# Optimization experiments

Measured on AMD Instinct MI355X. Metric: run time of the kernel, lower is better.

Reference implementation:

```python
import jax, jax.numpy as jnp
import numpy as np

VOC = 32000
D = 512          # embedding_dim == hidden_dim
POS = 1024       # position_embeddings_count


def _layernorm(x, gamma, beta, eps=1e-5):
    mu = jnp.mean(x, axis=-1, keepdims=True)
    var = jnp.var(x, axis=-1, keepdims=True)
    return (x - mu) * jax.lax.rsqrt(var + eps) * gamma + beta


def setup_inputs() -> dict:
    key = jax.random.key(0)
    ks = jax.random.split(key, 7)
    inp = jax.random.randint(ks[0], (32, 1024), 0, VOC)
    word_emb = jax.random.normal(ks[1], (VOC, D), dtype=jnp.float32) * 0.02
    pos_emb = jax.random.normal(ks[2], (POS, D), dtype=jnp.float32) * 0.02
    gamma = jnp.ones((D,), dtype=jnp.float32)
    beta = jnp.zeros((D,), dtype=jnp.float32)
    # torch.rand -> uniform [0,1) init in the original Attention module
    Wk = jax.random.uniform(ks[3], (D, D), dtype=jnp.float32)
    Wq = jax.random.uniform(ks[4], (D, D), dtype=jnp.float32)
    Wv = jax.random.uniform(ks[5], (D, D), dtype=jnp.float32)
    return {"input": inp, "word_emb": word_emb, "pos_emb": pos_emb,
            "gamma": gamma, "beta": beta, "Wk": Wk, "Wq": Wq, "Wv": Wv}


def reference(input, word_emb, pos_emb, gamma, beta, Wk, Wq, Wv):
    S = input.shape[-1]
    # MiniBertEmbedding: word + positional, then LayerNorm
    emb = word_emb[input] + pos_emb[:S][None, :, :]   # [B,S,D]
    x = _layernorm(emb, gamma, beta)
    # Attention: single-head QK^T softmax V with param matrices
    k = jnp.einsum('bsd,dh->bsh', x, Wk)
    q = jnp.einsum('bsd,dh->bsh', x, Wq)
    v = jnp.einsum('bsd,do->bso', x, Wv)
    qk = jnp.einsum('bqh,bkh->bqk', q, k) / jnp.sqrt(jnp.float32(D))
    attn = jax.nn.softmax(qk, axis=-1)
    return jnp.einsum('bqk,bko->bqo', attn, v)
```

## Files before the change

### kernel.cpp

```cpp
#include <hip/hip_runtime.h>
#include <math.h>

typedef _Float16 f16;
typedef _Float16 half8 __attribute__((ext_vector_type(8)));
typedef _Float16 hv2 __attribute__((ext_vector_type(2)));
typedef _Float16 hv4 __attribute__((ext_vector_type(4)));
typedef float f32x4 __attribute__((ext_vector_type(4)));
typedef __attribute__((address_space(1))) const unsigned int gu32;
typedef __attribute__((address_space(3))) unsigned int lu32;

#define BB 32
#define SS 1024
#define DD 512
#define NR (BB*SS)
#define CH 16

__device__ __forceinline__ void stage128(const char* g, int ldb, char* lds,
                                         int wv, int ln) {
  #pragma unroll
  for (int r = 0; r < 4; r++) {
    int slot = r * 256 + wv * 64 + ln;
    int row = slot >> 3, cp = slot & 7;
    int c = cp ^ (row & 7);
    const char* gp = g + (size_t)row * ldb + (c << 4);
    char* lp = lds + ((slot - ln) << 4);
    __builtin_amdgcn_global_load_lds((gu32*)gp, (lu32*)lp, 16, 0, 0);
  }
}

__device__ __forceinline__ void stage8k_512(const char* g, int ldb, char* lds) {
  int tid = threadIdx.x;
  int slot = tid;
  int row = slot >> 3, cp = slot & 7;
  int c = cp ^ (row & 7);
  const char* gp = g + (size_t)row * ldb + (c << 4);
  char* lp = lds + ((slot - (tid & 63)) << 4);
  __builtin_amdgcn_global_load_lds((gu32*)gp, (lu32*)lp, 16, 0, 0);
}

__device__ __forceinline__ void stage16k_512(const char* g, int ldb, char* lds) {
  int tid = threadIdx.x;
  #pragma unroll
  for (int r = 0; r < 2; r++) {
    int slot = r * 512 + tid;
    int row = slot >> 3, cp = slot & 7;
    int c = cp ^ (row & 7);
    const char* gp = g + (size_t)row * ldb + (c << 4);
    char* lp = lds + ((slot - (tid & 63)) << 4);
    __builtin_amdgcn_global_load_lds((gu32*)gp, (lu32*)lp, 16, 0, 0);
  }
}

__device__ __forceinline__ void stageB32(const f16* X, size_t rowbase, int k0,
                                         char* Bset) {
  int tid = threadIdx.x;
  int q4 = tid >> 7;
  int inner = tid & 127;
  char* lds = Bset + q4 * 4096;
  const char* g = (const char*)(X + (rowbase + (size_t)q4 * 256) * DD + k0);
  #pragma unroll
  for (int r = 0; r < 2; r++) {
    int slot = r * 128 + inner;
    int row = slot >> 3, cp = slot & 7;
    int c = cp ^ (row & 7);
    const char* gp = g + (size_t)row * 1024 + (c << 4);
    char* lp = lds + ((slot - (tid & 63)) << 4);
    __builtin_amdgcn_global_load_lds((gu32*)gp, (lu32*)lp, 16, 0, 0);
  }
}

__device__ __forceinline__ half8 frag_ld(const char* lds, int row, int kc) {
  return *(const half8*)(lds + row * 128 + ((kc ^ (row & 7)) << 4));
}

__device__ __forceinline__ f32x4 MF(half8 a, half8 b, f32x4 c) {
  return __builtin_amdgcn_mfma_f32_16x16x32_f16(a, b, c, 0, 0, 0);
}

__global__ __launch_bounds__(256) void k_prep(
    const int* __restrict__ inp, const float* __restrict__ wemb,
    const float* __restrict__ pemb, const float* __restrict__ gamma,
    const float* __restrict__ beta, f16* __restrict__ Xhi, f16* __restrict__ Xlo,
    const float* __restrict__ Wq, const float* __restrict__ Wk,
    const float* __restrict__ Wv, f16* __restrict__ Wqh, f16* __restrict__ Wql,
    f16* __restrict__ Wkh, f16* __restrict__ Wkl, f16* __restrict__ Wvt)
{
  int bid = blockIdx.x;
  int tid = threadIdx.x;
  __shared__ float red[10];
  __shared__ float Lt[64][65];
  if (bid >= NR) {
    int t  = bid - NR;
    int mz = t >> 6;
    int tt = t & 63;
    if (mz < 2) {
      const float* W = mz ? Wk : Wq;
      f16* Oh = mz ? Wkh : Wqh;
      f16* Ol = mz ? Wkl : Wql;
      #pragma unroll
      for (int p = 0; p < 4; p++) {
        size_t base = (size_t)tt * 4096 + p * 1024 + tid * 4;
        float4 v = *(const float4*)&W[base];
        f16 h0 = (f16)v.x, h1 = (f16)v.y, h2 = (f16)v.z, h3 = (f16)v.w;
        hv4 hi = {h0, h1, h2, h3};
        hv4 lo = {(f16)(v.x - (float)h0), (f16)(v.y - (float)h1),
                  (f16)(v.z - (float)h2), (f16)(v.w - (float)h3)};
        *(hv4*)&Oh[base] = hi;
        *(hv4*)&Ol[base] = lo;
      }
      return;
    }
    int tr = tt >> 3, tc = tt & 7;
    int rr = tid >> 4;
    int c4 = (tid & 15) * 4;
    #pragma unroll
    for (int p = 0; p < 4; p++) {
      float4 v = *(const float4*)&Wv[(size_t)(tr * 64 + p * 16 + rr) * DD + tc * 64 + c4];
      Lt[p * 16 + rr][c4 + 0] = v.x; Lt[p * 16 + rr][c4 + 1] = v.y;
      Lt[p * 16 + rr][c4 + 2] = v.z; Lt[p * 16 + rr][c4 + 3] = v.w;
    }
    __syncthreads();
    #pragma unroll
    for (int p = 0; p < 4; p++) {
      int dl = p * 16 + rr;
      float v0 = Lt[c4 + 0][dl], v1 = Lt[c4 + 1][dl];
      float v2 = Lt[c4 + 2][dl], v3 = Lt[c4 + 3][dl];
      size_t o = (size_t)(tc * 64 + dl) * DD + tr * 64 + c4;
      *(hv4*)&Wvt[o] = (hv4){(f16)v0, (f16)v1, (f16)v2, (f16)v3};
    }
    return;
  }
  int row = bid;
  int s   = row & (SS - 1);
  int tok = inp[row];
  float2 w = ((const float2*)(wemb + (size_t)tok * DD))[tid];
  float2 p = ((const float2*)(pemb + (size_t)s   * DD))[tid];
  float ex = w.x + p.x, ey = w.y + p.y;
  float sum = ex + ey, ssq = ex*ex + ey*ey;
  #pragma unroll
  for (int off = 32; off > 0; off >>= 1) {
    sum += __shfl_down(sum, off, 64);
    ssq += __shfl_down(ssq, off, 64);
  }
  int wv = tid >> 6, ln = tid & 63;
  if (ln == 0) { red[wv] = sum; red[4 + wv] = ssq; }
  __syncthreads();
  if (tid == 0) {
    float s4 = red[0] + red[1] + red[2] + red[3];
    float q4 = red[4] + red[5] + red[6] + red[7];
    float mean = s4 * (1.0f / DD);
    float var  = q4 * (1.0f / DD) - mean * mean;
    red[8] = mean; red[9] = rsqrtf(var + 1e-5f);
  }
  __syncthreads();
  float mean = red[8], rstd = red[9];
  float2 g  = ((const float2*)gamma)[tid];
  float2 bt = ((const float2*)beta)[tid];
  float ox = (ex - mean) * rstd * g.x + bt.x;
  float oy = (ey - mean) * rstd * g.y + bt.y;
  f16 hx = (f16)ox, hy = (f16)oy;
  f16 lx = (f16)(ox - (float)hx), ly = (f16)(oy - (float)hy);
  ((hv2*)(Xhi + (size_t)row * DD))[tid] = (hv2){hx, hy};
  ((hv2*)(Xlo + (size_t)row * DD))[tid] = (hv2){lx, ly};
}

__global__ __launch_bounds__(256, 2) void k_mt(
    const f16* __restrict__ Wkh, const f16* __restrict__ Wkl,
    const f16* __restrict__ Wqh, const f16* __restrict__ Wql,
    f16* __restrict__ Mthi, f16* __restrict__ Mtlo)
{
  __shared__ __align__(16) char Ah[16384], Al[16384], Bh[16384], Bl[16384];
  int tid = threadIdx.x, wv = tid >> 6, ln = tid & 63;
  int mw = wv & 1, nw = wv >> 1;
  int n0 = blockIdx.x * 128;
  int m0 = blockIdx.y * 128;
  f32x4 acc[4][4];
  #pragma unroll
  for (int i = 0; i < 4; i++)
    #pragma unroll
    for (int j = 0; j < 4; j++) acc[i][j] = (f32x4)(0.0f);
  int quad = ln >> 4, l15 = ln & 15;
  for (int k0 = 0; k0 < DD; k0 += 64) {
    __syncthreads();
    stage128((const char*)(Wkh + (size_t)m0 * DD + k0), 1024, Ah, wv, ln);
    stage128((const char*)(Wkl + (size_t)m0 * DD + k0), 1024, Al, wv, ln);
    stage128((const char*)(Wqh + (size_t)n0 * DD + k0), 1024, Bh, wv, ln);
    stage128((const char*)(Wql + (size_t)n0 * DD + k0), 1024, Bl, wv, ln);
    __syncthreads();
    #pragma unroll
    for (int ks = 0; ks < 2; ks++) {
      int kc = ks * 4 + quad;
      half8 ah[4], al[4], bh[4], bl[4];
      #pragma unroll
      for (int t = 0; t < 4; t++) {
        ah[t] = frag_ld(Ah, mw * 64 + t * 16 + l15, kc);
        al[t] = frag_ld(Al, mw * 64 + t * 16 + l15, kc);
        bh[t] = frag_ld(Bh, nw * 64 + t * 16 + l15, kc);
        bl[t] = frag_ld(Bl, nw * 64 + t * 16 + l15, kc);
      }
      #pragma unroll
      for (int i = 0; i < 4; i++)
        #pragma unroll
        for (int j = 0; j < 4; j++) {
          acc[i][j] = MF(ah[i], bh[j], acc[i][j]);
          acc[i][j] = MF(ah[i], bl[j], acc[i][j]);
          acc[i][j] = MF(al[i], bh[j], acc[i][j]);
        }
    }
  }
  #pragma unroll
  for (int i = 0; i < 4; i++)
    #pragma unroll
    for (int j = 0; j < 4; j++)
      #pragma unroll
      for (int rg = 0; rg < 4; rg++) {
        int gm = m0 + mw * 64 + i * 16 + quad * 4 + rg;
        int gn = n0 + nw * 64 + j * 16 + l15;
        size_t o = (size_t)gm * DD + gn;
        float v = acc[i][j][rg];
        f16 h = (f16)v;
        Mthi[o] = h; Mtlo[o] = (f16)(v - (float)h);
      }
}

__global__ __launch_bounds__(512, 4) void k_projm(
    const f16* __restrict__ Xhi, const f16* __restrict__ Xlo,
    const f16* __restrict__ Mthi, const f16* __restrict__ Mtlo,
    f16* __restrict__ Sqhi, f16* __restrict__ Sqlo)
{
  __shared__ __align__(16) char Ah[16384], Al[16384], Bh[16384], Bl[16384];
  int tid = threadIdx.x, wv = tid >> 6, ln = tid & 63;
  int mw = wv & 1, nw = wv >> 1;
  int L = blockIdx.x;
  int xb = (L >> 3) & 3;
  int y  = ((L >> 5) << 3) + (L & 7);
  int n0 = xb * 128;
  int m0 = y * 128;
  f32x4 acc[4][2];
  #pragma unroll
  for (int i = 0; i < 4; i++)
    #pragma unroll
    for (int j = 0; j < 2; j++) acc[i][j] = (f32x4)(0.0f);
  int quad = ln >> 4, l15 = ln & 15;
  for (int k0 = 0; k0 < DD; k0 += 64) {
    __syncthreads();
    stage16k_512((const char*)(Xhi  + (size_t)m0 * DD + k0), 1024, Ah);
    stage16k_512((const char*)(Xlo  + (size_t)m0 * DD + k0), 1024, Al);
    stage16k_512((const char*)(Mthi + (size_t)n0 * DD + k0), 1024, Bh);
    stage16k_512((const char*)(Mtlo + (size_t)n0 * DD + k0), 1024, Bl);
    __syncthreads();
    #pragma unroll
    for (int ks = 0; ks < 2; ks++) {
      int kc = ks * 4 + quad;
      half8 ah[4], al[4], bh[2], bl[2];
      #pragma unroll
      for (int t = 0; t < 4; t++) {
        ah[t] = frag_ld(Ah, mw * 64 + t * 16 + l15, kc);
        al[t] = frag_ld(Al, mw * 64 + t * 16 + l15, kc);
      }
      #pragma unroll
      for (int t = 0; t < 2; t++) {
        bh[t] = frag_ld(Bh, nw * 32 + t * 16 + l15, kc);
        bl[t] = frag_ld(Bl, nw * 32 + t * 16 + l15, kc);
      }
      #pragma unroll
      for (int i = 0; i < 4; i++)
        #pragma unroll
        for (int j = 0; j < 2; j++) {
          acc[i][j] = MF(ah[i], bh[j], acc[i][j]);
          acc[i][j] = MF(ah[i], bl[j], acc[i][j]);
          acc[i][j] = MF(al[i], bh[j], acc[i][j]);
        }
    }
  }
  #pragma unroll
  for (int i = 0; i < 4; i++)
    #pragma unroll
    for (int j = 0; j < 2; j++)
      #pragma unroll
      for (int rg = 0; rg < 4; rg++) {
        int gm = m0 + mw * 64 + i * 16 + quad * 4 + rg;
        int gn = n0 + nw * 32 + j * 16 + l15;
        size_t o = (size_t)gm * DD + gn;
        float v = acc[i][j][rg];
        f16 h = (f16)v;
        Sqhi[o] = h; Sqlo[o] = (f16)(v - (float)h);
      }
}

__global__ __launch_bounds__(256, 2) void k_vt(
    const f16* __restrict__ Wvt, const f16* __restrict__ Xhi, f16* __restrict__ Vt)
{
  __shared__ __align__(16) char Ah[2][16384], Bh[2][16384];
  int tid = threadIdx.x, wv = tid >> 6, ln = tid & 63;
  int mw = wv & 1, nw = wv >> 1;
  int orig = blockIdx.x;
  int L = (orig & 7) * 128 + (orig >> 3);
  int c = L >> 7, t = L & 127;
  int m0 = (t & 3) * 128;
  int n0 = (c * 32 + (t >> 2)) * 128;
  f32x4 acc[4][4];
  #pragma unroll
  for (int i = 0; i < 4; i++)
    #pragma unroll
    for (int j = 0; j < 4; j++) acc[i][j] = (f32x4)(0.0f);
  int quad = ln >> 4, l15 = ln & 15;
  stage128((const char*)(Wvt + (size_t)m0 * DD), 1024, Ah[0], wv, ln);
  stage128((const char*)(Xhi + (size_t)n0 * DD), 1024, Bh[0], wv, ln);
  for (int k0 = 0; k0 < DD; k0 += 64) {
    int cur = (k0 >> 6) & 1;
    __builtin_amdgcn_s_barrier();
    __builtin_amdgcn_sched_barrier(0);
    if (k0 + 64 < DD) {
      stage128((const char*)(Wvt + (size_t)m0 * DD + k0 + 64), 1024, Ah[cur ^ 1], wv, ln);
      stage128((const char*)(Xhi + (size_t)n0 * DD + k0 + 64), 1024, Bh[cur ^ 1], wv, ln);
      asm volatile("s_waitcnt vmcnt(8)" ::: "memory");
    } else {
      asm volatile("s_waitcnt vmcnt(0)" ::: "memory");
    }
    __builtin_amdgcn_s_barrier();
    __builtin_amdgcn_sched_barrier(0);
    #pragma unroll
    for (int ks = 0; ks < 2; ks++) {
      int kc = ks * 4 + quad;
      half8 a[4], b[4];
      #pragma unroll
      for (int tt = 0; tt < 4; tt++) {
        a[tt] = frag_ld(Ah[cur], mw * 64 + tt * 16 + l15, kc);
        b[tt] = frag_ld(Bh[cur], nw * 64 + tt * 16 + l15, kc);
      }
      #pragma unroll
      for (int i = 0; i < 4; i++)
        #pragma unroll
        for (int j = 0; j < 4; j++) acc[i][j] = MF(a[i], b[j], acc[i][j]);
    }
  }
  #pragma unroll
  for (int i = 0; i < 4; i++)
    #pragma unroll
    for (int j = 0; j < 4; j++)
      #pragma unroll
      for (int rg = 0; rg < 4; rg++) {
        int gm = m0 + mw * 64 + i * 16 + quad * 4 + rg;
        int gn = n0 + nw * 64 + j * 16 + l15;
        Vt[(size_t)gm * NR + gn] = (f16)acc[i][j][rg];
      }
}

__global__ __launch_bounds__(512, 2) void k_qk(
    const f16* __restrict__ Sqhi, const f16* __restrict__ Sqlo,
    const f16* __restrict__ Xhi, const f16* __restrict__ Xlo,
    f16* __restrict__ Pws, f16* __restrict__ Pd)
{
  __shared__ __align__(16) char Ah[8192], Al[8192];
  __shared__ __align__(16) char Bh[2][16384], Bl[2][16384];
  int tid = threadIdx.x, wv = tid >> 6, ln = tid & 63;
  int rowg = wv & 1, qd = wv >> 1;
  int L = blockIdx.x;
  int g  = L >> 7;
  int rr = L & 127;
  int z  = g * 8 + (rr & 7);
  int m0 = (rr >> 3) * 64;
  size_t zr = (size_t)z * SS;
  f32x4 acc[2][16];
  #pragma unroll
  for (int i = 0; i < 2; i++)
    #pragma unroll
    for (int j = 0; j < 16; j++) acc[i][j] = (f32x4)(0.0f);
  int quad = ln >> 4, l15 = ln & 15;

  stage8k_512((const char*)(Sqhi + (zr + m0) * DD), 1024, Ah);
  stage8k_512((const char*)(Sqlo + (zr + m0) * DD), 1024, Al);
  stageB32(Xhi, zr + 0, 0, Bh[0]);
  stageB32(Xlo, zr + 0, 0, Bl[0]);

  half8 afh[2][2], afl[2][2];
  for (int k0 = 0; k0 < DD; k0 += 64) {
    #pragma unroll
    for (int r = 0; r < 8; r++) {
      __builtin_amdgcn_s_barrier();
      __builtin_amdgcn_sched_barrier(0);
      bool lastPhase = (k0 == DD - 64 && r == 7);
      if (!lastPhase) {
        int nk0 = (r == 7) ? k0 + 64 : k0;
        int nr  = (r + 1) & 7;
        stageB32(Xhi, zr + nr * 32, nk0, Bh[(r + 1) & 1]);
        stageB32(Xlo, zr + nr * 32, nk0, Bl[(r + 1) & 1]);
        if (r == 7) {
          stage8k_512((const char*)(Sqhi + (zr + m0) * DD + k0 + 64), 1024, Ah);
          stage8k_512((const char*)(Sqlo + (zr + m0) * DD + k0 + 64), 1024, Al);
          asm volatile("s_waitcnt vmcnt(6)" ::: "memory");
        } else {
          asm volatile("s_waitcnt vmcnt(4)" ::: "memory");
        }
      } else {
        asm volatile("s_waitcnt vmcnt(0)" ::: "memory");
      }
      __builtin_amdgcn_s_barrier();
      __builtin_amdgcn_sched_barrier(0);
      if (r == 0) {
        #pragma unroll
        for (int ks = 0; ks < 2; ks++)
          #pragma unroll
          for (int i = 0; i < 2; i++) {
            afh[ks][i] = frag_ld(Ah, rowg * 32 + i * 16 + l15, ks * 4 + quad);
            afl[ks][i] = frag_ld(Al, rowg * 32 + i * 16 + l15, ks * 4 + quad);
          }
      }
      const char* Bhc = Bh[r & 1] + qd * 4096;
      const char* Blc = Bl[r & 1] + qd * 4096;
      #pragma unroll
      for (int ks = 0; ks < 2; ks++) {
        int kc = ks * 4 + quad;
        #pragma unroll
        for (int jj = 0; jj < 2; jj++) {
          half8 bh = frag_ld(Bhc, jj * 16 + l15, kc);
          half8 bl = frag_ld(Blc, jj * 16 + l15, kc);
          #pragma unroll
          for (int i = 0; i < 2; i++) {
            acc[i][r * 2 + jj] = MF(afh[ks][i], bh, acc[i][r * 2 + jj]);
            acc[i][r * 2 + jj] = MF(afh[ks][i], bl, acc[i][r * 2 + jj]);
            acc[i][r * 2 + jj] = MF(afl[ks][i], bh, acc[i][r * 2 + jj]);
          }
        }
      }
    }
  }
  __syncthreads();
  float* redm = (float*)&Bh[0][0];
  float* reds = redm + 256;

  const float scale = 0.044194173824159216f;
  float mx[2][4];
  #pragma unroll
  for (int i = 0; i < 2; i++)
    #pragma unroll
    for (int rg = 0; rg < 4; rg++) mx[i][rg] = -3.0e38f;
  #pragma unroll
  for (int i = 0; i < 2; i++)
    #pragma unroll
    for (int j = 0; j < 16; j++)
      #pragma unroll
      for (int rg = 0; rg < 4; rg++) {
        acc[i][j][rg] *= scale;
        mx[i][rg] = fmaxf(mx[i][rg], acc[i][j][rg]);
      }
  #pragma unroll
  for (int off = 1; off < 16; off <<= 1)
    #pragma unroll
    for (int i = 0; i < 2; i++)
      #pragma unroll
      for (int rg = 0; rg < 4; rg++)
        mx[i][rg] = fmaxf(mx[i][rg], __shfl_xor(mx[i][rg], off, 64));
  if (l15 == 0) {
    #pragma unroll
    for (int i = 0; i < 2; i++)
      #pragma unroll
      for (int rg = 0; rg < 4; rg++)
        redm[qd * 64 + rowg * 32 + i * 16 + quad * 4 + rg] = mx[i][rg];
  }
  __syncthreads();
  float fm[2][4], sum[2][4];
  #pragma unroll
  for (int i = 0; i < 2; i++)
    #pragma unroll
    for (int rg = 0; rg < 4; rg++) {
      int row = rowg * 32 + i * 16 + quad * 4 + rg;
      fm[i][rg] = fmaxf(fmaxf(redm[row], redm[64 + row]),
                        fmaxf(redm[128 + row], redm[192 + row]));
      sum[i][rg] = 0.0f;
    }
  #pragma unroll
  for (int i = 0; i < 2; i++)
    #pragma unroll
    for (int j = 0; j < 16; j++)
      #pragma unroll
      for (int rg = 0; rg < 4; rg++) {
        float e = __expf(acc[i][j][rg] - fm[i][rg]);
        acc[i][j][rg] = e;
        sum[i][rg] += e;
      }
  #pragma unroll
  for (int off = 1; off < 16; off <<= 1)
    #pragma unroll
    for (int i = 0; i < 2; i++)
      #pragma unroll
      for (int rg = 0; rg < 4; rg++)
        sum[i][rg] += __shfl_xor(sum[i][rg], off, 64);
  if (l15 == 0) {
    #pragma unroll
    for (int i = 0; i < 2; i++)
      #pragma unroll
      for (int rg = 0; rg < 4; rg++)
        reds[qd * 64 + rowg * 32 + i * 16 + quad * 4 + rg] = sum[i][rg];
  }
  __syncthreads();
  float inv[2][4];
  #pragma unroll
  for (int i = 0; i < 2; i++)
    #pragma unroll
    for (int rg = 0; rg < 4; rg++) {
      int row = rowg * 32 + i * 16 + quad * 4 + rg;
      inv[i][rg] = 1.0f / (reds[row] + reds[64 + row] + reds[128 + row] + reds[192 + row]);
    }
  f16* Pb = (z < CH) ? Pws : Pd;
  size_t zo = (size_t)((z < CH) ? z : z - CH);
  #pragma unroll
  for (int i = 0; i < 2; i++)
    #pragma unroll
    for (int j = 0; j < 16; j++)
      #pragma unroll
      for (int rg = 0; rg < 4; rg++) {
        int row = rowg * 32 + i * 16 + quad * 4 + rg;
        int col = qd * 256 + j * 16 + l15;
        Pb[(zo * SS + m0 + row) * SS + col] = (f16)(acc[i][j][rg] * inv[i][rg]);
      }
}

__global__ __launch_bounds__(256, 2) void k_pv(
    const f16* __restrict__ P, const f16* __restrict__ Vt, float* __restrict__ O,
    int zoff)
{
  __shared__ __align__(16) char Ah[2][16384], Bh[2][16384];
  int tid = threadIdx.x, wv = tid >> 6, ln = tid & 63;
  int mw = wv & 1, nw = wv >> 1;
  int orig = blockIdx.x;
  int L = (orig & 7) * 64 + (orig >> 3);
  int c = L >> 6, t = L & 63;
  int zl = 2 * c + (t >> 5);
  int m0 = ((t >> 2) & 7) * 128;
  int n0 = (t & 3) * 128;
  int b  = zoff + zl;
  const char* Pt = (const char*)(P + ((size_t)zl * SS + m0) * SS);
  const char* Vb = (const char*)(Vt + (size_t)n0 * NR + (size_t)b * SS);
  f32x4 acc[4][4];
  #pragma unroll
  for (int i = 0; i < 4; i++)
    #pragma unroll
    for (int j = 0; j < 4; j++) acc[i][j] = (f32x4)(0.0f);
  int quad = ln >> 4, l15 = ln & 15;
  stage128(Pt, 2048, Ah[0], wv, ln);
  stage128(Vb, NR * 2, Bh[0], wv, ln);
  for (int k0 = 0; k0 < SS; k0 += 64) {
    int cur = (k0 >> 6) & 1;
    __builtin_amdgcn_s_barrier();
    __builtin_amdgcn_sched_barrier(0);
    if (k0 + 64 < SS) {
      stage128(Pt + (k0 + 64) * 2, 2048, Ah[cur ^ 1], wv, ln);
      stage128(Vb + (k0 + 64) * 2, NR * 2, Bh[cur ^ 1], wv, ln);
      asm volatile("s_waitcnt vmcnt(8)" ::: "memory");
    } else {
      asm volatile("s_waitcnt vmcnt(0)" ::: "memory");
    }
    __builtin_amdgcn_s_barrier();
    __builtin_amdgcn_sched_barrier(0);
    #pragma unroll
    for (int ks = 0; ks < 2; ks++) {
      int kc = ks * 4 + quad;
      half8 a[4], bf[4];
      #pragma unroll
      for (int tt = 0; tt < 4; tt++) {
        a[tt]  = frag_ld(Ah[cur], mw * 64 + tt * 16 + l15, kc);
        bf[tt] = frag_ld(Bh[cur], nw * 64 + tt * 16 + l15, kc);
      }
      #pragma unroll
      for (int i = 0; i < 4; i++)
        #pragma unroll
        for (int j = 0; j < 4; j++) acc[i][j] = MF(a[i], bf[j], acc[i][j]);
    }
  }
  #pragma unroll
  for (int i = 0; i < 4; i++)
    #pragma unroll
    for (int j = 0; j < 4; j++)
      #pragma unroll
      for (int rg = 0; rg < 4; rg++) {
        int gm = m0 + mw * 64 + i * 16 + quad * 4 + rg;
        int gn = n0 + nw * 64 + j * 16 + l15;
        O[((size_t)b * SS + gm) * DD + gn] = acc[i][j][rg];
      }
}

extern "C" void kernel_launch(void* const* d_in, const int* in_sizes, int n_in,
                              void* d_out, int out_size, void* d_ws, size_t ws_size,
                              hipStream_t stream) {
  const int*   inp   = (const int*)d_in[0];
  const float* wemb  = (const float*)d_in[1];
  const float* pemb  = (const float*)d_in[2];
  const float* gamma = (const float*)d_in[3];
  const float* beta  = (const float*)d_in[4];
  const float* Wk    = (const float*)d_in[5];
  const float* Wq    = (const float*)d_in[6];
  const float* Wv    = (const float*)d_in[7];

  char* ws = (char*)d_ws;
  f16* Xhi  = (f16*)ws;
  f16* Xlo  = (f16*)(ws + ((size_t)32 << 20));
  f16* Sqhi = (f16*)(ws + ((size_t)64 << 20));
  f16* Sqlo = (f16*)(ws + ((size_t)96 << 20));
  f16* Vt   = (f16*)(ws + ((size_t)128 << 20));
  f16* Pws  = (f16*)(ws + ((size_t)160 << 20));
  f16* Pd   = (f16*)d_out;

  f16* Wqh  = (f16*)d_out;
  f16* Wql  = Wqh + (size_t)DD * DD;
  f16* Wkh  = Wql + (size_t)DD * DD;
  f16* Wkl  = Wkh + (size_t)DD * DD;
  f16* Wvt  = Wkl + (size_t)DD * DD;
  f16* Mthi = Wvt + (size_t)DD * DD;
  f16* Mtlo = Mthi + (size_t)DD * DD;

  k_prep<<<NR + 192, 256, 0, stream>>>(inp, wemb, pemb, gamma, beta, Xhi, Xlo,
                                       Wq, Wk, Wv, Wqh, Wql, Wkh, Wkl, Wvt);
  k_mt<<<dim3(DD / 128, DD / 128), 256, 0, stream>>>(Wkh, Wkl, Wqh, Wql, Mthi, Mtlo);
  k_projm<<<1024, 512, 0, stream>>>(Xhi, Xlo, Mthi, Mtlo, Sqhi, Sqlo);
  k_vt<<<1024, 256, 0, stream>>>(Wvt, Xhi, Vt);
  k_qk<<<512, 512, 0, stream>>>(Sqhi, Sqlo, Xhi, Xlo, Pws, Pd);
  k_pv<<<512, 256, 0, stream>>>(Pd,  Vt, (float*)d_out, CH);
  k_pv<<<512, 256, 0, stream>>>(Pws, Vt, (float*)d_out, 0);
}
```

Before: 425.8 us.

## Shrink QK+softmax tile to 32 query rows with 256-thread blocks

The fused QK^T+softmax kernel now uses 256-thread blocks covering 32 query rows instead of 512-thread blocks covering 64 rows, doubling the grid to 1024 blocks. Each wave stages its own slice of the key tiles, and softmax reductions get dedicated shared arrays instead of reusing the B buffers, which removes one __syncthreads. The aim is more, smaller blocks for better load balance and scheduling flexibility. In exchange, key (X) tiles are reloaded twice as often across blocks, and each wave has more outstanding loads per phase.

```diff
diff --git a/kernel.cpp b/kernel.cpp
--- a/kernel.cpp
+++ b/kernel.cpp
@@ -28,16 +28,6 @@
   }
 }
 
-__device__ __forceinline__ void stage8k_512(const char* g, int ldb, char* lds) {
-  int tid = threadIdx.x;
-  int slot = tid;
-  int row = slot >> 3, cp = slot & 7;
-  int c = cp ^ (row & 7);
-  const char* gp = g + (size_t)row * ldb + (c << 4);
-  char* lp = lds + ((slot - (tid & 63)) << 4);
-  __builtin_amdgcn_global_load_lds((gu32*)gp, (lu32*)lp, 16, 0, 0);
-}
-
 __device__ __forceinline__ void stage16k_512(const char* g, int ldb, char* lds) {
   int tid = threadIdx.x;
   #pragma unroll
@@ -51,20 +41,28 @@
   }
 }
 
-__device__ __forceinline__ void stageB32(const f16* X, size_t rowbase, int k0,
-                                         char* Bset) {
+__device__ __forceinline__ void stageA32(const f16* Sq, size_t rowbase, int k0,
+                                         char* lds) {
   int tid = threadIdx.x;
-  int q4 = tid >> 7;
-  int inner = tid & 127;
-  char* lds = Bset + q4 * 4096;
-  const char* g = (const char*)(X + (rowbase + (size_t)q4 * 256) * DD + k0);
-  #pragma unroll
-  for (int r = 0; r < 2; r++) {
-    int slot = r * 128 + inner;
+  int slot = tid;
+  int row = slot >> 3, cp = slot & 7;
+  int c = cp ^ (row & 7);
+  const char* gp = (const char*)(Sq + (rowbase + (size_t)row) * DD + k0) + (c << 4);
+  char* lp = lds + ((slot - (tid & 63)) << 4);
+  __builtin_amdgcn_global_load_lds((gu32*)gp, (lu32*)lp, 16, 0, 0);
+}
+
+__device__ __forceinline__ void stageB32w(const f16* X, size_t rowbase, int k0,
+                                          char* BsetQd) {
+  int ln = threadIdx.x & 63;
+  const char* g = (const char*)(X + rowbase * DD + k0);
+  #pragma unroll
+  for (int r = 0; r < 4; r++) {
+    int slot = r * 64 + ln;
     int row = slot >> 3, cp = slot & 7;
     int c = cp ^ (row & 7);
     const char* gp = g + (size_t)row * 1024 + (c << 4);
-    char* lp = lds + ((slot - (tid & 63)) << 4);
+    char* lp = BsetQd + ((slot - ln) << 4);
     __builtin_amdgcn_global_load_lds((gu32*)gp, (lu32*)lp, 16, 0, 0);
   }
 }
@@ -347,21 +345,23 @@
       }
 }
 
-__global__ __launch_bounds__(512, 2) void k_qk(
+__global__ __launch_bounds__(256, 2) void k_qk(
     const f16* __restrict__ Sqhi, const f16* __restrict__ Sqlo,
     const f16* __restrict__ Xhi, const f16* __restrict__ Xlo,
     f16* __restrict__ Pws, f16* __restrict__ Pd)
 {
-  __shared__ __align__(16) char Ah[8192], Al[8192];
+  __shared__ __align__(16) char Ah[4096], Al[4096];
   __shared__ __align__(16) char Bh[2][16384], Bl[2][16384];
-  int tid = threadIdx.x, wv = tid >> 6, ln = tid & 63;
-  int rowg = wv & 1, qd = wv >> 1;
+  __shared__ float redm[4][32], reds[4][32];
+  int tid = threadIdx.x, ln = tid & 63;
+  int qd = tid >> 6;
   int L = blockIdx.x;
-  int g  = L >> 7;
-  int rr = L & 127;
+  int g  = L >> 8;
+  int rr = L & 255;
   int z  = g * 8 + (rr & 7);
-  int m0 = (rr >> 3) * 64;
+  int m0 = (rr >> 3) * 32;
   size_t zr = (size_t)z * SS;
+  size_t kb = zr + (size_t)qd * 256;
   f32x4 acc[2][16];
   #pragma unroll
   for (int i = 0; i < 2; i++)
@@ -369,10 +369,10 @@
     for (int j = 0; j < 16; j++) acc[i][j] = (f32x4)(0.0f);
   int quad = ln >> 4, l15 = ln & 15;
 
-  stage8k_512((const char*)(Sqhi + (zr + m0) * DD), 1024, Ah);
-  stage8k_512((const char*)(Sqlo + (zr + m0) * DD), 1024, Al);
-  stageB32(Xhi, zr + 0, 0, Bh[0]);
-  stageB32(Xlo, zr + 0, 0, Bl[0]);
+  stageA32(Sqhi, zr + m0, 0, Ah);
+  stageA32(Sqlo, zr + m0, 0, Al);
+  stageB32w(Xhi, kb, 0, Bh[0] + qd * 4096);
+  stageB32w(Xlo, kb, 0, Bl[0] + qd * 4096);
 
   half8 afh[2][2], afl[2][2];
   for (int k0 = 0; k0 < DD; k0 += 64) {
@@ -384,14 +384,14 @@
       if (!lastPhase) {
         int nk0 = (r == 7) ? k0 + 64 : k0;
         int nr  = (r + 1) & 7;
-        stageB32(Xhi, zr + nr * 32, nk0, Bh[(r + 1) & 1]);
-        stageB32(Xlo, zr + nr * 32, nk0, Bl[(r + 1) & 1]);
+        stageB32w(Xhi, kb + nr * 32, nk0, Bh[(r + 1) & 1] + qd * 4096);
+        stageB32w(Xlo, kb + nr * 32, nk0, Bl[(r + 1) & 1] + qd * 4096);
         if (r == 7) {
-          stage8k_512((const char*)(Sqhi + (zr + m0) * DD + k0 + 64), 1024, Ah);
-          stage8k_512((const char*)(Sqlo + (zr + m0) * DD + k0 + 64), 1024, Al);
-          asm volatile("s_waitcnt vmcnt(6)" ::: "memory");
+          stageA32(Sqhi, zr + m0, k0 + 64, Ah);
+          stageA32(Sqlo, zr + m0, k0 + 64, Al);
+          asm volatile("s_waitcnt vmcnt(10)" ::: "memory");
         } else {
-          asm volatile("s_waitcnt vmcnt(4)" ::: "memory");
+          asm volatile("s_waitcnt vmcnt(8)" ::: "memory");
         }
       } else {
         asm volatile("s_waitcnt vmcnt(0)" ::: "memory");
@@ -403,8 +403,8 @@
         for (int ks = 0; ks < 2; ks++)
           #pragma unroll
           for (int i = 0; i < 2; i++) {
-            afh[ks][i] = frag_ld(Ah, rowg * 32 + i * 16 + l15, ks * 4 + quad);
-            afl[ks][i] = frag_ld(Al, rowg * 32 + i * 16 + l15, ks * 4 + quad);
+            afh[ks][i] = frag_ld(Ah, i * 16 + l15, ks * 4 + quad);
+            afl[ks][i] = frag_ld(Al, i * 16 + l15, ks * 4 + quad);
           }
       }
       const char* Bhc = Bh[r & 1] + qd * 4096;
@@ -426,9 +426,6 @@
       }
     }
   }
-  __syncthreads();
-  float* redm = (float*)&Bh[0][0];
-  float* reds = redm + 256;
 
   const float scale = 0.044194173824159216f;
   float mx[2][4];
@@ -457,7 +454,7 @@
     for (int i = 0; i < 2; i++)
       #pragma unroll
       for (int rg = 0; rg < 4; rg++)
-        redm[qd * 64 + rowg * 32 + i * 16 + quad * 4 + rg] = mx[i][rg];
+        redm[qd][i * 16 + quad * 4 + rg] = mx[i][rg];
   }
   __syncthreads();
   float fm[2][4], sum[2][4];
@@ -465,9 +462,9 @@
   for (int i = 0; i < 2; i++)
     #pragma unroll
     for (int rg = 0; rg < 4; rg++) {
-      int row = rowg * 32 + i * 16 + quad * 4 + rg;
-      fm[i][rg] = fmaxf(fmaxf(redm[row], redm[64 + row]),
-                        fmaxf(redm[128 + row], redm[192 + row]));
+      int row = i * 16 + quad * 4 + rg;
+      fm[i][rg] = fmaxf(fmaxf(redm[0][row], redm[1][row]),
+                        fmaxf(redm[2][row], redm[3][row]));
       sum[i][rg] = 0.0f;
     }
   #pragma unroll
@@ -492,7 +489,7 @@
     for (int i = 0; i < 2; i++)
       #pragma unroll
       for (int rg = 0; rg < 4; rg++)
-        reds[qd * 64 + rowg * 32 + i * 16 + quad * 4 + rg] = sum[i][rg];
+        reds[qd][i * 16 + quad * 4 + rg] = sum[i][rg];
   }
   __syncthreads();
   float inv[2][4];
@@ -500,8 +497,8 @@
   for (int i = 0; i < 2; i++)
     #pragma unroll
     for (int rg = 0; rg < 4; rg++) {
-      int row = rowg * 32 + i * 16 + quad * 4 + rg;
-      inv[i][rg] = 1.0f / (reds[row] + reds[64 + row] + reds[128 + row] + reds[192 + row]);
+      int row = i * 16 + quad * 4 + rg;
+      inv[i][rg] = 1.0f / (reds[0][row] + reds[1][row] + reds[2][row] + reds[3][row]);
     }
   f16* Pb = (z < CH) ? Pws : Pd;
   size_t zo = (size_t)((z < CH) ? z : z - CH);
@@ -511,7 +508,7 @@
     for (int j = 0; j < 16; j++)
       #pragma unroll
       for (int rg = 0; rg < 4; rg++) {
-        int row = rowg * 32 + i * 16 + quad * 4 + rg;
+        int row = i * 16 + quad * 4 + rg;
         int col = qd * 256 + j * 16 + l15;
         Pb[(zo * SS + m0 + row) * SS + col] = (f16)(acc[i][j][rg] * inv[i][rg]);
       }
@@ -615,7 +612,7 @@
   k_mt<<<dim3(DD / 128, DD / 128), 256, 0, stream>>>(Wkh, Wkl, Wqh, Wql, Mthi, Mtlo);
   k_projm<<<1024, 512, 0, stream>>>(Xhi, Xlo, Mthi, Mtlo, Sqhi, Sqlo);
   k_vt<<<1024, 256, 0, stream>>>(Wvt, Xhi, Vt);
-  k_qk<<<512, 512, 0, stream>>>(Sqhi, Sqlo, Xhi, Xlo, Pws, Pd);
+  k_qk<<<1024, 256, 0, stream>>>(Sqhi, Sqlo, Xhi, Xlo, Pws, Pd);
   k_pv<<<512, 256, 0, stream>>>(Pd,  Vt, (float*)d_out, CH);
   k_pv<<<512, 256, 0, stream>>>(Pws, Vt, (float*)d_out, 0);
 }
```

After: 416.2 us. 2.2% less time.
